# Performance work log

Measured on AMD Instinct MI355X. Metric: run time of the kernel, lower is better.

Reference implementation:

```python
import jax, jax.numpy as jnp
import numpy as np

N = 16384
HID = 256
MI = 128
POS_PER_NODE = 4
TEMP = 0.5


def setup_inputs() -> dict:
    key = jax.random.key(0)
    k1, k2, k3, k4 = jax.random.split(key, 4)
    h_v1 = jax.random.normal(k1, (N, HID), dtype=jnp.float32)
    h_v2 = jax.random.normal(k2, (N, HID), dtype=jnp.float32)
    W = jax.random.normal(k3, (HID, MI), dtype=jnp.float32) * (1.0 / np.sqrt(HID))
    b = jnp.zeros((MI,), dtype=jnp.float32)
    # 4 positives per row -> every row has a nonzero positive count
    pos_row = jnp.repeat(jnp.arange(N, dtype=jnp.int32), POS_PER_NODE)
    pos_col = jax.random.randint(k4, (N * POS_PER_NODE,), 0, N, dtype=jnp.int32)
    return {"h_v1": h_v1, "h_v2": h_v2, "W": W, "b": b,
            "pos_row": pos_row, "pos_col": pos_col}


def _l2norm(x):
    return x / jnp.linalg.norm(x, axis=-1, keepdims=True)


def _cal_loss_mi(e1, e2, pos_row, pos_col):
    # sim_mat[i,j] = <e1_i, e2_j> / T   (N x N, the big intermediate)
    sim = jnp.einsum('ik,jk->ij', e1, e2) / TEMP
    sim = sim - jax.lax.stop_gradient(jnp.max(sim, axis=1, keepdims=True))
    sim = jnp.exp(sim)
    sim_pos = sim[pos_row, pos_col]                      # [E] gather
    row_sum = jnp.sum(sim, axis=1)                       # [N]
    pos_sum = jax.ops.segment_sum(sim_pos, pos_row, num_segments=N)
    denom = (row_sum - pos_sum)[pos_row]                 # [E]
    log_lv = jnp.log(sim_pos / denom)                    # [E]
    pos_cnt = jax.ops.segment_sum(jnp.ones_like(sim_pos), pos_row, num_segments=N)
    per_row = jax.ops.segment_sum(log_lv, pos_row, num_segments=N) / pos_cnt
    return -jnp.mean(per_row)


def reference(h_v1, h_v2, W, b, pos_row, pos_col):
    p1 = _l2norm(jax.nn.relu(h_v1 @ W + b))
    p2 = _l2norm(jax.nn.relu(h_v2 @ W + b))
    loss = 0.5 * (_cal_loss_mi(p1, p2, pos_row, pos_col)
                  + _cal_loss_mi(p2, p1, pos_row, pos_col))
    return loss
```

## Files before the change

### kernel.cpp

```cpp
#include <hip/hip_runtime.h>

typedef unsigned short ushort_t;
typedef unsigned int uint32;
typedef __attribute__((ext_vector_type(8))) short short8;
typedef __attribute__((ext_vector_type(4))) float f32x4;
typedef __attribute__((ext_vector_type(2))) float f32x2;

#define HID 256
#define MI 128
#define ALPHA 2.8853900817779268f
#define LN2F 0.69314718055994531f

__device__ __forceinline__ float bflo(uint32 u) { return __uint_as_float(u << 16); }
__device__ __forceinline__ float bfhi(uint32 u) { return __uint_as_float(u & 0xffff0000u); }
__device__ __forceinline__ ushort_t f2bf(float f) {
  uint32 u = __float_as_uint(f);
  u += 0x7fffu + ((u >> 16) & 1u);
  return (ushort_t)(u >> 16);
}

__global__ __launch_bounds__(256) void prep_kernel(
    const float* __restrict__ W, ushort_t* __restrict__ Wtb,
    float* __restrict__ fbase, int nz, float* __restrict__ out)
{
  int idx = blockIdx.x * 256 + threadIdx.x;
  if (idx < HID * MI) {
    int k = idx >> 7, nn = idx & 127;
    Wtb[nn * HID + k] = f2bf(W[k * MI + nn]);
  }
  if (idx < nz) fbase[idx] = 0.f;
  if (idx == 0) out[0] = 0.f;
}

__global__ __launch_bounds__(256) void proj_kernel(
    const float* __restrict__ h1, const float* __restrict__ h2,
    const ushort_t* __restrict__ Wtb, const float* __restrict__ b,
    ushort_t* __restrict__ p1b, ushort_t* __restrict__ p2b, int n)
{
  __shared__ __align__(16) unsigned char hb[64 * 512];
  int t = threadIdx.x;
  int lane = t & 63, w = t >> 6;
  int lr = lane & 15, lg = lane >> 4;
  long R0 = (long)blockIdx.x * 64;
  const float* src = (R0 < n) ? (h1 + R0 * HID) : (h2 + (R0 - n) * HID);
  ushort_t* dst = (R0 < n) ? (p1b + R0 * MI) : (p2b + (R0 - n) * MI);
  float scale = (R0 < n) ? ALPHA : 1.0f;

  float bb[8];
  #pragma unroll
  for (int ch = 0; ch < 8; ++ch) bb[ch] = b[ch * 16 + lr];

  const float4* g4 = (const float4*)src;
  #pragma unroll
  for (int i = 0; i < 16; ++i) {
    int idx4 = i * 256 + t;
    float4 v = g4[idx4];
    int row = idx4 >> 6;
    int k0 = (idx4 & 63) * 4;
    int gr = k0 >> 3;
    int off = row * 512 + ((gr ^ (row & 15)) << 4) + (k0 & 7) * 2;
    uint32 lo = (uint32)f2bf(v.x) | ((uint32)f2bf(v.y) << 16);
    uint32 hi = (uint32)f2bf(v.z) | ((uint32)f2bf(v.w) << 16);
    uint2 pk; pk.x = lo; pk.y = hi;
    *(uint2*)(hb + off) = pk;
  }
  __syncthreads();

  short8 afr[8];
  #pragma unroll
  for (int kt = 0; kt < 8; ++kt) {
    int row = w * 16 + lr;
    int g = kt * 4 + lg;
    afr[kt] = *(const short8*)(hb + row * 512 + ((g ^ (row & 15)) << 4));
  }

  f32x4 acc[8];
  #pragma unroll
  for (int ch = 0; ch < 8; ++ch) acc[ch] = (f32x4){0.f, 0.f, 0.f, 0.f};
  #pragma unroll
  for (int ch = 0; ch < 8; ++ch) {
    #pragma unroll
    for (int kt = 0; kt < 8; ++kt) {
      short8 bf = *(const short8*)(Wtb + (size_t)(ch * 16 + lr) * HID + kt * 32 + lg * 8);
      acc[ch] = __builtin_amdgcn_mfma_f32_16x16x32_bf16(afr[kt], bf, acc[ch], 0, 0, 0);
    }
  }

  #pragma unroll
  for (int r = 0; r < 4; ++r) {
    float v[8];
    float ss = 0.f;
    #pragma unroll
    for (int ch = 0; ch < 8; ++ch) {
      v[ch] = fmaxf(acc[ch][r] + bb[ch], 0.f);
      ss += v[ch] * v[ch];
    }
    ss += __shfl_xor(ss, 1, 64);
    ss += __shfl_xor(ss, 2, 64);
    ss += __shfl_xor(ss, 4, 64);
    ss += __shfl_xor(ss, 8, 64);
    float rn = rsqrtf(ss) * scale;
    int row = w * 16 + lg * 4 + r;
    #pragma unroll
    for (int ch = 0; ch < 8; ++ch)
      dst[(size_t)row * MI + ch * 16 + lr] = f2bf(v[ch] * rn);
  }
}

__global__ __launch_bounds__(256, 2) void sim_kernel(
    const ushort_t* __restrict__ p1b, const ushort_t* __restrict__ p2b,
    float* __restrict__ rowsum, float* __restrict__ colsum,
    const int* __restrict__ pos_row, const int* __restrict__ pos_col,
    float* __restrict__ psum1, float* __restrict__ psum2,
    float* __restrict__ srow1, float* __restrict__ srow2,
    float* __restrict__ cntb, int E)
{
  __shared__ __align__(16) unsigned char ldsB[32768];
  __shared__ float colacc[1024];
  int t = threadIdx.x;
  int lane = t & 63, w = t >> 6;
  int lr = lane & 15, lg = lane >> 4;
  int rowbase = blockIdx.y * 256 + w * 64;
  int jbase = blockIdx.x * 1024;

  uint4 st0, st1, st2, st3;
  int gs = t & 15, r0 = t >> 4;
  int sw = (gs ^ (r0 & 15)) << 4;

  auto load_stage = [&](int jt) {
    int j0 = jbase + jt * 64;
    const ushort_t* base = p2b + (size_t)(j0 + r0) * MI + (gs << 3);
    st0 = *(const uint4*)(base);
    st1 = *(const uint4*)(base + 16 * MI);
    st2 = *(const uint4*)(base + 32 * MI);
    st3 = *(const uint4*)(base + 48 * MI);
  };
  auto write_stage = [&](int buf) {
    unsigned char* base = ldsB + buf * 16384 + r0 * 256 + sw;
    *(uint4*)(base)            = st0;
    *(uint4*)(base + 16 * 256) = st1;
    *(uint4*)(base + 32 * 256) = st2;
    *(uint4*)(base + 48 * 256) = st3;
  };

  load_stage(0);

  short8 afr[4][4];
  #pragma unroll
  for (int rt = 0; rt < 4; ++rt)
    #pragma unroll
    for (int kt = 0; kt < 4; ++kt)
      afr[rt][kt] = *(const short8*)(p1b + (size_t)(rowbase + rt * 16 + lr) * MI + kt * 32 + lg * 8);

  colacc[t] = 0.f;
  colacc[256 + t] = 0.f;
  colacc[512 + t] = 0.f;
  colacc[768 + t] = 0.f;

  f32x2 rs2[4][2];
  #pragma unroll
  for (int rt = 0; rt < 4; ++rt) {
    rs2[rt][0] = (f32x2){0.f, 0.f};
    rs2[rt][1] = (f32x2){0.f, 0.f};
  }

  write_stage(0);
  __syncthreads();

  for (int jt = 0; jt < 16; ++jt) {
    int cur = jt & 1;
    if (jt + 1 < 16) load_stage(jt + 1);
    const unsigned char* B = ldsB + cur * 16384;

    #pragma unroll
    for (int ch = 0; ch < 4; ++ch) {
      f32x4 acc[4];
      #pragma unroll
      for (int rt = 0; rt < 4; ++rt) acc[rt] = (f32x4){0.f, 0.f, 0.f, 0.f};
      #pragma unroll
      for (int kt = 0; kt < 4; ++kt) {
        int ncol = ch * 16 + lr;
        int g = kt * 4 + lg;
        short8 bf = *(const short8*)(B + ncol * 256 + ((g ^ (ncol & 15)) << 4));
        #pragma unroll
        for (int rt = 0; rt < 4; ++rt)
          acc[rt] = __builtin_amdgcn_mfma_f32_16x16x32_bf16(afr[rt][kt], bf, acc[rt], 0, 0, 0);
      }
      f32x2 cs2 = (f32x2){0.f, 0.f};
      #pragma unroll
      for (int rt = 0; rt < 4; ++rt) {
        f32x2 e01, e23;
        e01[0] = __builtin_amdgcn_exp2f(acc[rt][0]);
        e01[1] = __builtin_amdgcn_exp2f(acc[rt][1]);
        e23[0] = __builtin_amdgcn_exp2f(acc[rt][2]);
        e23[1] = __builtin_amdgcn_exp2f(acc[rt][3]);
        rs2[rt][0] += e01;
        rs2[rt][1] += e23;
        cs2 += e01;
        cs2 += e23;
      }
      float csum = cs2[0] + cs2[1];
      csum += __shfl_xor(csum, 16, 64);
      csum += __shfl_xor(csum, 32, 64);
      if (lg == 0) atomicAdd(&colacc[jt * 64 + ch * 16 + lr], csum);
    }
    if (jt + 1 < 16) write_stage(1 - cur);
    __syncthreads();
  }

  #pragma unroll
  for (int rt = 0; rt < 4; ++rt)
    #pragma unroll
    for (int j = 0; j < 2; ++j)
      #pragma unroll
      for (int s = 0; s < 2; ++s) {
        float v = rs2[rt][j][s];
        v += __shfl_xor(v, 1, 64);
        v += __shfl_xor(v, 2, 64);
        v += __shfl_xor(v, 4, 64);
        v += __shfl_xor(v, 8, 64);
        if (lr == 0) atomicAdd(&rowsum[rowbase + rt * 16 + lg * 4 + j * 2 + s], v);
      }

  atomicAdd(&colsum[jbase + t], colacc[t]);
  atomicAdd(&colsum[jbase + 256 + t], colacc[256 + t]);
  atomicAdd(&colsum[jbase + 512 + t], colacc[512 + t]);
  atomicAdd(&colsum[jbase + 768 + t], colacc[768 + t]);

  {
    int eb = blockIdx.y * gridDim.x + blockIdx.x;
    int e = eb * 64 + (t >> 2), q = t & 3;
    if (e < E) {
      int r = pos_row[e], c = pos_col[e];
      const uint4* a1 = (const uint4*)(p1b + (size_t)r * MI) + q * 4;
      const uint4* b1 = (const uint4*)(p2b + (size_t)c * MI) + q * 4;
      const uint4* a2 = (const uint4*)(p1b + (size_t)c * MI) + q * 4;
      const uint4* b2 = (const uint4*)(p2b + (size_t)r * MI) + q * 4;
      float d1 = 0.f, d2 = 0.f;
      #pragma unroll
      for (int it = 0; it < 4; ++it) {
        uint4 x = a1[it], y = b1[it];
        d1 += bflo(x.x) * bflo(y.x) + bfhi(x.x) * bfhi(y.x);
        d1 += bflo(x.y) * bflo(y.y) + bfhi(x.y) * bfhi(y.y);
        d1 += bflo(x.z) * bflo(y.z) + bfhi(x.z) * bfhi(y.z);
        d1 += bflo(x.w) * bflo(y.w) + bfhi(x.w) * bfhi(y.w);
        uint4 u = a2[it], v = b2[it];
        d2 += bflo(u.x) * bflo(v.x) + bfhi(u.x) * bfhi(v.x);
        d2 += bflo(u.y) * bflo(v.y) + bfhi(u.y) * bfhi(v.y);
        d2 += bflo(u.z) * bflo(v.z) + bfhi(u.z) * bfhi(v.z);
        d2 += bflo(u.w) * bflo(v.w) + bfhi(u.w) * bfhi(v.w);
      }
      d1 += __shfl_xor(d1, 1, 64);
      d1 += __shfl_xor(d1, 2, 64);
      d2 += __shfl_xor(d2, 1, 64);
      d2 += __shfl_xor(d2, 2, 64);
      if (q == 0) {
        float e1 = __builtin_amdgcn_exp2f(d1);
        float e2 = __builtin_amdgcn_exp2f(d2);
        atomicAdd(&psum1[r], e1);
        atomicAdd(&srow1[r], d1 * LN2F);
        atomicAdd(&psum2[r], e2);
        atomicAdd(&srow2[r], d2 * LN2F);
        atomicAdd(&cntb[r], 1.0f);
      }
    }
  }
}

__global__ __launch_bounds__(256) void finalize_kernel(
    const float* __restrict__ rowsum, const float* __restrict__ colsum,
    const float* __restrict__ psum1, const float* __restrict__ psum2,
    const float* __restrict__ srow1, const float* __restrict__ srow2,
    const float* __restrict__ cntb, float* __restrict__ out, int n)
{
  __shared__ float sred[4];
  int r = blockIdx.x * 256 + threadIdx.x;
  float local = 0.f;
  if (r < n) {
    float inv = 1.0f / cntb[r];
    float d1 = rowsum[r] - psum1[r];
    float d2 = colsum[r] - psum2[r];
    local = srow1[r] * inv - __builtin_amdgcn_logf(d1) * LN2F
          + srow2[r] * inv - __builtin_amdgcn_logf(d2) * LN2F;
  }
  #pragma unroll
  for (int m = 1; m <= 32; m <<= 1) local += __shfl_xor(local, m, 64);
  int lane = threadIdx.x & 63, wv = threadIdx.x >> 6;
  if (lane == 0) sred[wv] = local;
  __syncthreads();
  if (threadIdx.x == 0) {
    float tot = sred[0] + sred[1] + sred[2] + sred[3];
    atomicAdd(out, -tot / (2.0f * n));
  }
}

extern "C" void kernel_launch(void* const* d_in, const int* in_sizes, int n_in,
                              void* d_out, int out_size, void* d_ws, size_t ws_size,
                              hipStream_t stream)
{
  const float* h1 = (const float*)d_in[0];
  const float* h2 = (const float*)d_in[1];
  const float* W  = (const float*)d_in[2];
  const float* b  = (const float*)d_in[3];
  const int* pos_row = (const int*)d_in[4];
  const int* pos_col = (const int*)d_in[5];
  int n = in_sizes[0] / HID;
  int E = in_sizes[4];
  float* out = (float*)d_out;

  char* ws = (char*)d_ws;
  ushort_t* p1b = (ushort_t*)ws;
  ushort_t* p2b = p1b + (size_t)n * MI;
  float* fbase  = (float*)(ws + (size_t)2 * n * MI * sizeof(ushort_t));
  float* rowsum = fbase;
  float* colsum = rowsum + n;
  float* psum1  = colsum + n;
  float* psum2  = psum1 + n;
  float* srow1  = psum2 + n;
  float* srow2  = srow1 + n;
  float* cntb   = srow2 + n;
  ushort_t* Wtb = (ushort_t*)(cntb + n);

  int nz = 7 * n;
  prep_kernel<<<(nz + 255) / 256, 256, 0, stream>>>(W, Wtb, fbase, nz, out);
  proj_kernel<<<2 * n / 64, 256, 0, stream>>>(h1, h2, Wtb, b, p1b, p2b, n);
  dim3 g2(n / 1024, n / 256);
  sim_kernel<<<g2, 256, 0, stream>>>(p1b, p2b, rowsum, colsum,
                                     pos_row, pos_col, psum1, psum2,
                                     srow1, srow2, cntb, E);
  finalize_kernel<<<(n + 255) / 256, 256, 0, stream>>>(rowsum, colsum, psum1, psum2,
                                                       srow1, srow2, cntb, out, n);
}
```

Before: 193.1 us.

## Fuse finalize into sim kernel via ticket counter and raise MFMA priority

Removes the separate finalize kernel launch. The last 64 sim blocks to finish (by atomic ticket) spin until every block has incremented the done counter, then each computes the per-row loss for 256 rows and atomically adds it to the output. It also wraps the MFMA loop in s_setprio so matrix issue gets scheduling priority over other waves. The spin-wait depends on all blocks eventually running, and it keeps up to 64 blocks occupied while they wait.

```diff
diff --git a/kernel.cpp b/kernel.cpp
--- a/kernel.cpp
+++ b/kernel.cpp
@@ -113,10 +113,13 @@
     const int* __restrict__ pos_row, const int* __restrict__ pos_col,
     float* __restrict__ psum1, float* __restrict__ psum2,
     float* __restrict__ srow1, float* __restrict__ srow2,
-    float* __restrict__ cntb, int E)
+    float* __restrict__ cntb, int E,
+    int* __restrict__ donecnt, float* __restrict__ out, int nrows)
 {
   __shared__ __align__(16) unsigned char ldsB[32768];
   __shared__ float colacc[1024];
+  __shared__ int ticket_s;
+  __shared__ float sred[4];
   int t = threadIdx.x;
   int lane = t & 63, w = t >> 6;
   int lr = lane & 15, lg = lane >> 4;
@@ -177,6 +180,7 @@
       f32x4 acc[4];
       #pragma unroll
       for (int rt = 0; rt < 4; ++rt) acc[rt] = (f32x4){0.f, 0.f, 0.f, 0.f};
+      __builtin_amdgcn_s_setprio(1);
       #pragma unroll
       for (int kt = 0; kt < 4; ++kt) {
         int ncol = ch * 16 + lr;
@@ -186,6 +190,7 @@
         for (int rt = 0; rt < 4; ++rt)
           acc[rt] = __builtin_amdgcn_mfma_f32_16x16x32_bf16(afr[rt][kt], bf, acc[rt], 0, 0, 0);
       }
+      __builtin_amdgcn_s_setprio(0);
       f32x2 cs2 = (f32x2){0.f, 0.f};
       #pragma unroll
       for (int rt = 0; rt < 4; ++rt) {
@@ -265,32 +270,31 @@
       }
     }
   }
-}
-
-__global__ __launch_bounds__(256) void finalize_kernel(
-    const float* __restrict__ rowsum, const float* __restrict__ colsum,
-    const float* __restrict__ psum1, const float* __restrict__ psum2,
-    const float* __restrict__ srow1, const float* __restrict__ srow2,
-    const float* __restrict__ cntb, float* __restrict__ out, int n)
-{
-  __shared__ float sred[4];
-  int r = blockIdx.x * 256 + threadIdx.x;
-  float local = 0.f;
-  if (r < n) {
+
+  int total = (int)(gridDim.x * gridDim.y);
+  int nfin = nrows >> 8;
+  __threadfence();
+  if (t == 0) ticket_s = atomicAdd(donecnt, 1);
+  __syncthreads();
+  int ticket = ticket_s;
+  if (ticket >= total - nfin) {
+    if (t == 0) {
+      while (atomicAdd(donecnt, 0) < total) { }
+    }
+    __syncthreads();
+    __threadfence();
+    int r = (ticket - (total - nfin)) * 256 + t;
     float inv = 1.0f / cntb[r];
     float d1 = rowsum[r] - psum1[r];
     float d2 = colsum[r] - psum2[r];
-    local = srow1[r] * inv - __builtin_amdgcn_logf(d1) * LN2F
-          + srow2[r] * inv - __builtin_amdgcn_logf(d2) * LN2F;
-  }
-  #pragma unroll
-  for (int m = 1; m <= 32; m <<= 1) local += __shfl_xor(local, m, 64);
-  int lane = threadIdx.x & 63, wv = threadIdx.x >> 6;
-  if (lane == 0) sred[wv] = local;
-  __syncthreads();
-  if (threadIdx.x == 0) {
-    float tot = sred[0] + sred[1] + sred[2] + sred[3];
-    atomicAdd(out, -tot / (2.0f * n));
+    float local = srow1[r] * inv - __builtin_amdgcn_logf(d1) * LN2F
+                + srow2[r] * inv - __builtin_amdgcn_logf(d2) * LN2F;
+    #pragma unroll
+    for (int m = 1; m <= 32; m <<= 1) local += __shfl_xor(local, m, 64);
+    if ((t & 63) == 0) sred[t >> 6] = local;
+    __syncthreads();
+    if (t == 0)
+      atomicAdd(out, -(sred[0] + sred[1] + sred[2] + sred[3]) / (2.0f * nrows));
   }
 }
 
@@ -319,15 +323,15 @@
   float* srow1  = psum2 + n;
   float* srow2  = srow1 + n;
   float* cntb   = srow2 + n;
-  ushort_t* Wtb = (ushort_t*)(cntb + n);
-
-  int nz = 7 * n;
+  int*   donecnt = (int*)(cntb + n);
+  ushort_t* Wtb = (ushort_t*)(cntb + n + 16);
+
+  int nz = 7 * n + 16;
   prep_kernel<<<(nz + 255) / 256, 256, 0, stream>>>(W, Wtb, fbase, nz, out);
   proj_kernel<<<2 * n / 64, 256, 0, stream>>>(h1, h2, Wtb, b, p1b, p2b, n);
   dim3 g2(n / 1024, n / 256);
   sim_kernel<<<g2, 256, 0, stream>>>(p1b, p2b, rowsum, colsum,
                                      pos_row, pos_col, psum1, psum2,
-                                     srow1, srow2, cntb, E);
-  finalize_kernel<<<(n + 255) / 256, 256, 0, stream>>>(rowsum, colsum, psum1, psum2,
-                                                       srow1, srow2, cntb, out, n);
-}
+                                     srow1, srow2, cntb, E,
+                                     donecnt, out, n);
+}
```

After: 281.0 us. +45.5%, slower.
